# Kernel optimization log

Hardware: AMD Instinct MI355X
Metric: run time of the kernel (lower is better)

Reference implementation:

```python
import jax, jax.numpy as jnp
import numpy as np

HID = 128      # hidden_features
NF = 32        # noise_features
NPL = NF // 4  # noise features per layer
RES = 512      # noise grid resolution
N = 262144     # number of query points


def leaky_relu(x):
    return jax.nn.leaky_relu(x, negative_slope=0.01)


def sample_bilinear(image, coords):
    """image: [M, H, W]; coords: [..., M, 2] -> [..., M]"""
    M, Hn, Wn = image.shape
    x = coords[..., 0] - 0.5
    y = coords[..., 1] - 0.5
    x0f = jnp.floor(x)
    y0f = jnp.floor(y)
    xw = x - x0f
    yw = y - y0f
    x0 = x0f.astype(jnp.int32) % Wn
    x1 = (x0f.astype(jnp.int32) + 1) % Wn
    y0 = y0f.astype(jnp.int32) % Hn
    y1 = (y0f.astype(jnp.int32) + 1) % Hn
    f = jnp.arange(M)  # broadcasts against [..., M] index arrays
    i00 = image[f, y0, x0]
    i01 = image[f, y0, x1]
    i10 = image[f, y1, x0]
    i11 = image[f, y1, x1]
    i0 = i00 + (i01 - i00) * xw
    i1 = i10 + (i11 - i10) * xw
    return i0 + (i1 - i0) * yw


def setup_inputs() -> dict:
    key = jax.random.key(0)
    ks = jax.random.split(key, 12)
    noise = jax.random.normal(ks[0], (NF, RES, RES), dtype=jnp.float32)
    coords = jax.random.normal(ks[1], (N, 2), dtype=jnp.float32)
    # NoiseTransforms param: randn * 0.05 * 2**i per feature
    scale = 0.05 * (2.0 ** np.arange(NF)).astype(np.float32)
    transformations = jax.random.normal(ks[2], (NF, 2, 2), dtype=jnp.float32) * scale[:, None, None]
    input_vec = jnp.ones((HID,), dtype=jnp.float32)
    s_lin = 1.0 / np.sqrt(HID)
    s_noise = 1.0 / np.sqrt(NPL)
    lw = jax.random.uniform(ks[3], (4, HID, HID), jnp.float32, -s_lin, s_lin)
    lb = jax.random.uniform(ks[4], (4, HID), jnp.float32, -s_lin, s_lin)
    lnw = jax.random.uniform(ks[5], (4, HID, NPL), jnp.float32, -s_noise, s_noise)
    tw1 = jax.random.uniform(ks[6], (HID, HID), jnp.float32, -s_lin, s_lin)
    tb1 = jax.random.uniform(ks[7], (HID,), jnp.float32, -s_lin, s_lin)
    tw2 = jax.random.uniform(ks[8], (1, HID), jnp.float32, -s_lin, s_lin)
    tb2 = jax.random.uniform(ks[9], (1,), jnp.float32, -s_lin, s_lin)
    return {"noise": noise, "coords": coords, "transformations": transformations,
            "input_vec": input_vec, "lw": lw, "lb": lb, "lnw": lnw,
            "tw1": tw1, "tb1": tb1, "tw2": tw2, "tb2": tb2}


def reference(noise, coords, transformations, input_vec, lw, lb, lnw, tw1, tb1, tw2, tb2):
    # noise coords: [..., NF, 2]
    noise_coords = jnp.einsum('...n,Mmn->...Mm', coords, transformations)
    noise_values = sample_bilinear(noise, noise_coords)  # [..., NF]
    x = input_vec  # [HID], broadcasts up through layer adds
    for i in range(4):
        nv = noise_values[..., i * NPL:(i + 1) * NPL]
        x = leaky_relu(jnp.einsum('...h,oh->...o', x, lw[i]) + lb[i]
                       + jnp.einsum('...n,on->...o', nv, lnw[i]))
    h = leaky_relu(jnp.einsum('...h,oh->...o', x, tw1) + tb1)
    return jnp.einsum('...h,oh->...o', h, tw2) + tb2  # [..., 1]
```

## Files before the change

### kernel.cpp

```cpp
#include <hip/hip_runtime.h>

typedef _Float16 f16;
typedef f16 f16x4 __attribute__((ext_vector_type(4)));
typedef f16 f16x8 __attribute__((ext_vector_type(8)));
typedef float f32x4 __attribute__((ext_vector_type(4)));

#define RES 512
#define PTS 128
#define XS  136
#define AS  16


__global__ __launch_bounds__(256)
void pack_w_k(const float* __restrict__ lw,  const float* __restrict__ lnw,
              const float* __restrict__ lb,  const float* __restrict__ tw1,
              const float* __restrict__ tb1,
              f16* __restrict__ wf, f16* __restrict__ waugf) {
    const int g = blockIdx.x * 256 + threadIdx.x;
    if (g < 10240) {
        const int L = g >> 11, r = g & 2047;
        const int lane = r & 63, frag = r >> 6;
        const int q = lane >> 4, l15 = lane & 15;
        const int mt = frag >> 2, c = frag & 3;
        const float* src = ((L < 4) ? (lw + L * 16384) : tw1)
                           + (mt * 16 + l15) * 128 + c * 32 + q * 8;
        f16x8 h;
        #pragma unroll
        for (int j = 0; j < 8; ++j) h[j] = (f16)src[j];
        *(f16x8*)(wf + (size_t)g * 8) = h;
    } else {
        const int ga = g - 10240;
        const int L = ga >> 9, r = ga & 511;
        const int lane = r & 63, mt = r >> 6;
        const int q = lane >> 4, l15 = lane & 15;
        const int row = mt * 16 + l15;
        f16x8 h = {};
        if (q == 0 && L < 4) {
            const float* src = lnw + L * 1024 + row * 8;
            #pragma unroll
            for (int j = 0; j < 8; ++j) h[j] = (f16)src[j];
        }
        if (q == 1)
            h[0] = (f16)((L < 4) ? lb[L * 128 + row] : tb1[row]);
        *(f16x8*)(waugf + (size_t)ga * 8) = h;
    }
}

__global__ __launch_bounds__(256, 8)
void sample_kernel(const float* __restrict__ noise,
                   const float* __restrict__ coords,
                   const float* __restrict__ trans,
                   f16* __restrict__ nv_ws, const int Ntot)
{
    __shared__ float T_sh[128];
    const int t = threadIdx.x;
    if (t < 128) T_sh[t] = trans[t];
    __syncthreads();

    const int g = blockIdx.x & 7;
    const int p = (blockIdx.x >> 3) * 256 + t;

    const float2 c2 = *(const float2*)(coords + p * 2);

    float nvr[4];
    {
        #pragma clang fp contract(off)
        const float cx = c2.x;
        const float cy = c2.y;
        #pragma unroll
        for (int k = 0; k < 4; ++k) {
            const int m = k * 8 + g;
            const float T00 = T_sh[m*4+0], T01 = T_sh[m*4+1];
            const float T10 = T_sh[m*4+2], T11 = T_sh[m*4+3];
            const float p0x = T00 * cx;
            const float p0y = T10 * cx;
            const float ncx = __builtin_fmaf(T01, cy, p0x);
            const float ncy = __builtin_fmaf(T11, cy, p0y);
            const float u = ncx - 0.5f;
            const float v = ncy - 0.5f;
            const float xf = floorf(u), yf = floorf(v);
            const float xw = u - xf, yw = v - yf;
            int ix = (xf >= 2147483648.0f || xf < -2147483648.0f) ? (int)(-2147483647 - 1) : (int)xf;
            int iy = (yf >= 2147483648.0f || yf < -2147483648.0f) ? (int)(-2147483647 - 1) : (int)yf;
            const int x0 = ix & (RES - 1);
            const int x1 = (int)(((unsigned)ix + 1u) & (unsigned)(RES - 1));
            const int y0 = iy & (RES - 1);
            const int y1 = (int)(((unsigned)iy + 1u) & (unsigned)(RES - 1));
            const float* pl = noise + m * (RES * RES);
            const float i00 = pl[y0 * RES + x0];
            const float i01 = pl[y0 * RES + x1];
            const float i10 = pl[y1 * RES + x0];
            const float i11 = pl[y1 * RES + x1];
            const float a0 = i00 + (i01 - i00) * xw;
            const float a1 = i10 + (i11 - i10) * xw;
            nvr[k] = a0 + (a1 - a0) * yw;
        }
    }
    #pragma unroll
    for (int k = 0; k < 4; ++k)
        nv_ws[(size_t)(g * 4 + k) * Ntot + p] = (f16)nvr[k];
}

__global__ __launch_bounds__(256, 2)
void mlp_kernel(const f16* __restrict__ nv_ws,
                const f16* __restrict__ wf,
                const f16* __restrict__ waugf,
                const float* __restrict__ input_vec,
                const float* __restrict__ tw2,
                const float* __restrict__ tb2,
                float* __restrict__ out, const int Ntot)
{
    __shared__ f16 Wm[16384];
    __shared__ f16 Waug[4096];
    __shared__ f16 xa[PTS * XS];
    __shared__ f16 xaug[PTS * AS];
    __shared__ __align__(16) float tw2_sh[128];

    const int t    = threadIdx.x;
    const int wave = t >> 6;
    const int lane = t & 63;
    const int q    = lane >> 4;
    const int l15  = lane & 15;
    const int pbase = blockIdx.x * PTS;
    const int pw    = wave * 32;
    const int p = t >> 1, h = t & 1;

    if (t < 128) {
        tw2_sh[t] = tw2[t];
        xaug[t * AS + 8] = (f16)1.0f;
        #pragma unroll
        for (int c = 9; c < 16; ++c) xaug[t * AS + c] = (f16)0.0f;
    }
    {
        #pragma unroll
        for (int j = 0; j < 8; ++j) {
            const float4 a = ((const float4*)input_vec)[h * 16 + j * 2];
            const float4 b = ((const float4*)input_vec)[h * 16 + j * 2 + 1];
            f16x8 hv;
            hv[0]=(f16)a.x; hv[1]=(f16)a.y; hv[2]=(f16)a.z; hv[3]=(f16)a.w;
            hv[4]=(f16)b.x; hv[5]=(f16)b.y; hv[6]=(f16)b.z; hv[7]=(f16)b.w;
            *(f16x8*)&xa[p * XS + h * 64 + j * 8] = hv;
        }
    }
    const float tb2_0 = tb2[0];

    f16x8 nva, nvb;
    {
        const int P = pbase + p;
        #pragma unroll
        for (int j = 0; j < 8; ++j) {
            nva[j] = nv_ws[(size_t)(j * 4 + 2 * h)     * Ntot + P];
            nvb[j] = nv_ws[(size_t)(j * 4 + 2 * h + 1) * Ntot + P];
        }
    }
    if (h == 0) *(f16x8*)&xaug[p * AS] = nva;

    f32x4 acc[2][8];
    #pragma unroll 1
    for (int L = 0; L < 5; ++L) {
        __syncthreads();
        {
            const f16* wsrc = wf + L * 16384;
            #pragma unroll
            for (int i = 0; i < 8; ++i) {
                const int idx = t + i * 256;
                *(f16x8*)&Wm[idx * 8] = *(const f16x8*)&wsrc[idx * 8];
            }
            const f16* asrc = waugf + L * 4096;
            *(f16x8*)&Waug[t * 8]         = *(const f16x8*)&asrc[t * 8];
            *(f16x8*)&Waug[(t + 256) * 8] = *(const f16x8*)&asrc[(t + 256) * 8];
        }
        __syncthreads();

        {
            const f32x4 z4 = {0.f, 0.f, 0.f, 0.f};
            #pragma unroll
            for (int i = 0; i < 2; ++i)
                #pragma unroll
                for (int mt = 0; mt < 8; ++mt) acc[i][mt] = z4;
        }
        const int pr0 = (pw + l15) * XS, pr1 = (pw + 16 + l15) * XS;
        #pragma unroll
        for (int c = 0; c < 4; ++c) {
            const int kc = c * 32 + q * 8;
            const f16x8 xb0 = *(const f16x8*)&xa[pr0 + kc];
            const f16x8 xb1 = *(const f16x8*)&xa[pr1 + kc];
            #pragma unroll
            for (int mt = 0; mt < 8; ++mt) {
                const f16x8 aw = *(const f16x8*)&Wm[((mt * 4 + c) * 64 + lane) * 8];
                acc[0][mt] = __builtin_amdgcn_mfma_f32_16x16x32_f16(aw, xb0, acc[0][mt], 0, 0, 0);
                acc[1][mt] = __builtin_amdgcn_mfma_f32_16x16x32_f16(aw, xb1, acc[1][mt], 0, 0, 0);
            }
        }
        {
            f16x8 xb0 = {}, xb1 = {};
            if (q < 2) {
                xb0 = *(const f16x8*)&xaug[(pw + l15) * AS + q * 8];
                xb1 = *(const f16x8*)&xaug[(pw + 16 + l15) * AS + q * 8];
            }
            #pragma unroll
            for (int mt = 0; mt < 8; ++mt) {
                const f16x8 aw = *(const f16x8*)&Waug[(mt * 64 + lane) * 8];
                acc[0][mt] = __builtin_amdgcn_mfma_f32_16x16x32_f16(aw, xb0, acc[0][mt], 0, 0, 0);
                acc[1][mt] = __builtin_amdgcn_mfma_f32_16x16x32_f16(aw, xb1, acc[1][mt], 0, 0, 0);
            }
        }

        if (L < 4) {
            #pragma unroll
            for (int i = 0; i < 2; ++i) {
                const int pr = (pw + i * 16 + l15) * XS;
                #pragma unroll
                for (int mt = 0; mt < 8; ++mt) {
                    f16x4 hv;
                    #pragma unroll
                    for (int r = 0; r < 4; ++r) {
                        float v = acc[i][mt][r];
                        v = fmaxf(v, 0.01f * v);
                        hv[r] = (f16)v;
                    }
                    *(f16x4*)&xa[pr + mt * 16 + q * 4] = hv;
                }
            }
            if (L < 3) {
                const int Ln = L + 1;
                if ((Ln >> 1) == h)
                    *(f16x8*)&xaug[p * AS] = (Ln & 1) ? nvb : nva;
            }
        } else {
            #pragma unroll
            for (int i = 0; i < 2; ++i) {
                float s = 0.f;
                #pragma unroll
                for (int mt = 0; mt < 8; ++mt) {
                    const f32x4 w4 = *(const f32x4*)&tw2_sh[mt * 16 + q * 4];
                    #pragma unroll
                    for (int r = 0; r < 4; ++r) {
                        float v = acc[i][mt][r];
                        v = fmaxf(v, 0.01f * v);
                        s += w4[r] * v;
                    }
                }
                s += __shfl_xor(s, 16);
                s += __shfl_xor(s, 32);
                if (q == 0) out[pbase + pw + i * 16 + l15] = s + tb2_0;
            }
        }
    }
}

extern "C" void kernel_launch(void* const* d_in, const int* in_sizes, int n_in,
                              void* d_out, int out_size, void* d_ws, size_t ws_size,
                              hipStream_t stream) {
    const float* noise  = (const float*)d_in[0];
    const float* coords = (const float*)d_in[1];
    const float* trans  = (const float*)d_in[2];
    const float* ivec   = (const float*)d_in[3];
    const float* lw     = (const float*)d_in[4];
    const float* lb     = (const float*)d_in[5];
    const float* lnw    = (const float*)d_in[6];
    const float* tw1    = (const float*)d_in[7];
    const float* tb1    = (const float*)d_in[8];
    const float* tw2    = (const float*)d_in[9];
    const float* tb2    = (const float*)d_in[10];
    float* o            = (float*)d_out;

    const int N = in_sizes[1] / 2;
    f16* nv    = (f16*)d_ws;
    const size_t NV = (size_t)N * 32 * sizeof(f16);
    f16* wfp   = (f16*)((char*)d_ws + NV);
    f16* waugp = wfp + 5 * 16384;

    pack_w_k<<<50, 256, 0, stream>>>(lw, lnw, lb, tw1, tb1, wfp, waugp);
    sample_kernel<<<(N / 256) * 8, 256, 0, stream>>>(noise, coords, trans, nv, N);
    mlp_kernel<<<N / PTS, 256, 0, stream>>>(nv, wfp, waugp, ivec, tw2, tb2, o, N);
}
```

Baseline: 231.7 us.

## Repack noise grid into fp16 2x2 quads and rebalance feature assignment across blocks

Adds a pre-pass that converts the fp32 noise planes into fp16 2x2 quad blocks, so each bilinear tap in the sampler reads 8 bytes from a smaller, more cache-friendly footprint. It also reassigns features to the 8 block groups so that cheap low-frequency and expensive high-frequency features are mixed evenly, balancing the random-access cost across groups. This adds a full pass over the 32 MB noise tensor on every call and reduces the precision of the noise samples to fp16 before interpolation. The old fp32 path is kept as a fallback when the workspace is too small.

```diff
diff --git a/kernel.cpp b/kernel.cpp
--- a/kernel.cpp
+++ b/kernel.cpp
@@ -10,6 +10,18 @@
 #define XS  136
 #define AS  16
 
+
+__global__ __launch_bounds__(256)
+void pack_quad_k(const float* __restrict__ n, f16* __restrict__ q) {
+    const int idx = blockIdx.x * 256 + threadIdx.x;
+    const int qx = idx & 255, rest = idx >> 8;
+    const int qy = rest & 255, m = rest >> 8;
+    const float* src = n + ((size_t)m * 512 + 2 * qy) * 512 + 2 * qx;
+    const float2 r0 = *(const float2*)(src);
+    const float2 r1 = *(const float2*)(src + 512);
+    f16x4 o; o[0]=(f16)r0.x; o[1]=(f16)r0.y; o[2]=(f16)r1.x; o[3]=(f16)r1.y;
+    *(f16x4*)(q + (size_t)idx * 4) = o;
+}
 
 __global__ __launch_bounds__(256)
 void pack_w_k(const float* __restrict__ lw,  const float* __restrict__ lnw,
@@ -46,8 +58,16 @@
     }
 }
 
+__device__ __forceinline__ float quad_tap(uint2 q, int sy, int sx) {
+    unsigned w = sy ? q.y : q.x;
+    w >>= (sx << 4);
+    union { unsigned short u; f16 h; } cv; cv.u = (unsigned short)w;
+    return (float)cv.h;
+}
+
+template <bool QUAD>
 __global__ __launch_bounds__(256, 8)
-void sample_kernel(const float* __restrict__ noise,
+void sample_kernel(const void* __restrict__ noise_v,
                    const float* __restrict__ coords,
                    const float* __restrict__ trans,
                    f16* __restrict__ nv_ws, const int Ntot)
@@ -60,6 +80,10 @@
     const int g = blockIdx.x & 7;
     const int p = (blockIdx.x >> 3) * 256 + t;
 
+    int mk[4];
+    if (g < 7) { mk[0] = g; mk[1] = g + 9; mk[2] = g + 17; mk[3] = g + 25; }
+    else       { mk[0] = 7; mk[1] = 8;     mk[2] = 16;     mk[3] = 24;     }
+
     const float2 c2 = *(const float2*)(coords + p * 2);
 
     float nvr[4];
@@ -69,7 +93,7 @@
         const float cy = c2.y;
         #pragma unroll
         for (int k = 0; k < 4; ++k) {
-            const int m = k * 8 + g;
+            const int m = mk[k];
             const float T00 = T_sh[m*4+0], T01 = T_sh[m*4+1];
             const float T10 = T_sh[m*4+2], T11 = T_sh[m*4+3];
             const float p0x = T00 * cx;
@@ -86,19 +110,39 @@
             const int x1 = (int)(((unsigned)ix + 1u) & (unsigned)(RES - 1));
             const int y0 = iy & (RES - 1);
             const int y1 = (int)(((unsigned)iy + 1u) & (unsigned)(RES - 1));
-            const float* pl = noise + m * (RES * RES);
-            const float i00 = pl[y0 * RES + x0];
-            const float i01 = pl[y0 * RES + x1];
-            const float i10 = pl[y1 * RES + x0];
-            const float i11 = pl[y1 * RES + x1];
+            float i00, i01, i10, i11;
+            if constexpr (QUAD) {
+                const f16* pl = (const f16*)noise_v + (size_t)m * (256 * 256 * 4);
+                const int qx0 = x0 >> 1, sx0 = x0 & 1;
+                const int qx1 = x1 >> 1, sx1 = x1 & 1;
+                const int qy0 = y0 >> 1, sy0 = y0 & 1;
+                const int qy1 = y1 >> 1, sy1 = y1 & 1;
+                const uint2 qa = *(const uint2*)(pl + (qy0 * 256 + qx0) * 4);
+                const uint2 qb = *(const uint2*)(pl + (qy0 * 256 + qx1) * 4);
+                const uint2 qc = *(const uint2*)(pl + (qy1 * 256 + qx0) * 4);
+                const uint2 qd = *(const uint2*)(pl + (qy1 * 256 + qx1) * 4);
+                i00 = quad_tap(qa, sy0, sx0);
+                i01 = quad_tap(qb, sy0, sx1);
+                i10 = quad_tap(qc, sy1, sx0);
+                i11 = quad_tap(qd, sy1, sx1);
+            } else {
+                const float* pl = (const float*)noise_v + (size_t)m * (RES * RES);
+                i00 = pl[y0 * RES + x0];
+                i01 = pl[y0 * RES + x1];
+                i10 = pl[y1 * RES + x0];
+                i11 = pl[y1 * RES + x1];
+            }
             const float a0 = i00 + (i01 - i00) * xw;
             const float a1 = i10 + (i11 - i10) * xw;
             nvr[k] = a0 + (a1 - a0) * yw;
         }
     }
     #pragma unroll
-    for (int k = 0; k < 4; ++k)
-        nv_ws[(size_t)(g * 4 + k) * Ntot + p] = (f16)nvr[k];
+    for (int k = 0; k < 4; ++k) {
+        const int m = mk[k];
+        const int slot = (m & 7) * 4 + (m >> 3);
+        nv_ws[(size_t)slot * Ntot + p] = (f16)nvr[k];
+    }
 }
 
 __global__ __launch_bounds__(256, 2)
@@ -267,11 +311,19 @@
 
     const int N = in_sizes[1] / 2;
     f16* nv    = (f16*)d_ws;
-    const size_t NV = (size_t)N * 32 * sizeof(f16);
-    f16* wfp   = (f16*)((char*)d_ws + NV);
+    const size_t NV = (size_t)N * 32;
+    f16* wfp   = nv + NV;
     f16* waugp = wfp + 5 * 16384;
+    f16* qn    = waugp + 5 * 4096;
+    const size_t need_full = (NV + 5 * 16384 + 5 * 4096
+                              + (size_t)32 * 256 * 256 * 4) * sizeof(f16);
 
     pack_w_k<<<50, 256, 0, stream>>>(lw, lnw, lb, tw1, tb1, wfp, waugp);
-    sample_kernel<<<(N / 256) * 8, 256, 0, stream>>>(noise, coords, trans, nv, N);
+    if (ws_size >= need_full) {
+        pack_quad_k<<<(32 * 256 * 256) / 256, 256, 0, stream>>>(noise, qn);
+        sample_kernel<true><<<(N / 256) * 8, 256, 0, stream>>>(qn, coords, trans, nv, N);
+    } else {
+        sample_kernel<false><<<(N / 256) * 8, 256, 0, stream>>>(noise, coords, trans, nv, N);
+    }
     mlp_kernel<<<N / PTS, 256, 0, stream>>>(nv, wfp, waugp, ivec, tw2, tb2, o, N);
 }
```

Result: no change. 235.5 us (+1.7%).
